# Kernel optimization log

Measured on AMD Instinct MI355X. Metric: run time of the kernel, lower is better.

Reference implementation:

```python
import jax, jax.numpy as jnp
import numpy as np

B, N = 2, 65536
V, VSUB, J, R = 6890, 689, 24, 64
THRESH = 0.12


def trilinear(grid, coords):
    # grid: [C, D, H, W]; coords: [..., 3] in [-1, 1] (x->W, y->H, z->D)
    C, D, H, W = grid.shape
    cs = jnp.clip(coords.reshape(-1, 3), -1.0, 1.0)
    x = (cs[:, 0] + 1.0) * 0.5 * (W - 1)
    y = (cs[:, 1] + 1.0) * 0.5 * (H - 1)
    z = (cs[:, 2] + 1.0) * 0.5 * (D - 1)
    x0 = jnp.floor(x).astype(jnp.int32); x1 = jnp.minimum(x0 + 1, W - 1)
    y0 = jnp.floor(y).astype(jnp.int32); y1 = jnp.minimum(y0 + 1, H - 1)
    z0 = jnp.floor(z).astype(jnp.int32); z1 = jnp.minimum(z0 + 1, D - 1)
    fx = x - x0; fy = y - y0; fz = z - z0
    g = lambda zi, yi, xi: grid[:, zi, yi, xi]  # [C, M]
    out = (g(z0, y0, x0) * ((1 - fz) * (1 - fy) * (1 - fx))
         + g(z0, y0, x1) * ((1 - fz) * (1 - fy) * fx)
         + g(z0, y1, x0) * ((1 - fz) * fy * (1 - fx))
         + g(z0, y1, x1) * ((1 - fz) * fy * fx)
         + g(z1, y0, x0) * (fz * (1 - fy) * (1 - fx))
         + g(z1, y0, x1) * (fz * (1 - fy) * fx)
         + g(z1, y1, x0) * (fz * fy * (1 - fx))
         + g(z1, y1, x1) * (fz * fy * fx))
    return out.T.reshape(coords.shape[:-1] + (C,))


def setup_inputs() -> dict:
    key = jax.random.key(0)
    ks = jax.random.split(key, 8)
    pts_in = jax.random.normal(ks[0], (B, N, 3), jnp.float32) * 0.4
    vs_template = jax.random.normal(ks[1], (1, VSUB, 3), jnp.float32) * 0.4
    shape_offset = jax.random.normal(ks[2], (1, V, 3), jnp.float32) * 0.01
    init_idx = jax.random.randint(ks[3], (N, 3), 0, V, jnp.int32)
    bar = jax.random.uniform(ks[4], (N, 3), jnp.float32) + 1e-3
    init_bar = bar / jnp.sum(bar, -1, keepdims=True)
    lbs_voxel = jax.nn.softmax(jax.random.normal(ks[5], (J, R, R, R), jnp.float32), axis=0)
    tfs = jnp.tile(jnp.eye(4, dtype=jnp.float32), (B, J, 1, 1)) \
        + 0.05 * jax.random.normal(ks[6], (B, J, 4, 4), jnp.float32)
    grid_scale = jnp.full((3,), 1.5, jnp.float32)
    grid_offset = jnp.zeros((3,), jnp.float32)
    return dict(pts_in=pts_in, vs_template=vs_template, shape_offset=shape_offset,
                init_idx=init_idx, init_bar=init_bar, lbs_voxel=lbs_voxel,
                tfs=tfs, grid_scale=grid_scale, grid_offset=grid_offset)


def reference(pts_in, vs_template, shape_offset, init_idx, init_bar, lbs_voxel, tfs, grid_scale, grid_offset):
    # --- KNN (K=1) against subsampled template vertices ---
    v = vs_template[0]  # [VSUB, 3]
    d2 = (jnp.sum(pts_in * pts_in, -1, keepdims=True)
          + jnp.sum(v * v, -1)[None, None, :]
          - 2.0 * jnp.einsum('bnd,vd->bnv', pts_in, v))  # [B,N,VSUB]
    dist_sq = jnp.min(d2, axis=-1)  # [B,N]
    mask = (dist_sq < THRESH ** 2)[..., None]  # [B,N,1]
    # --- barycentric interpolation of per-vertex shape offsets ---
    tri = shape_offset[0][init_idx]               # [N,3,3]
    off = jnp.sum(init_bar[..., None] * tri, -2)  # [N,3]
    pts = pts_in + off[None]
    # --- query LBS weights from explicit voxel grid (fast-SNARF) ---
    pts_norm = (pts - grid_offset) * grid_scale
    w = trilinear(lbs_voxel, pts_norm)  # [B,N,J]
    w = w / jnp.clip(jnp.sum(w, -1, keepdims=True), 1e-6, None)
    # --- forward skinning ---
    w_tf = jnp.einsum('bnj,bjkl->bnkl', w, tfs)  # [B,N,4,4]
    pts_h = jnp.concatenate([pts, jnp.ones_like(pts[..., :1])], -1)  # [B,N,4]
    pts_posed = jnp.einsum('bnkl,bnl->bnk', w_tf, pts_h)[..., :3]
    pts_cano_all = pts_posed.reshape(B, N, 1, 3)
    return pts_cano_all, mask, w_tf
```

## Files before the change

kernel.cpp:

```cpp
#include <hip/hip_runtime.h>
#include <math.h>

#define NB    2
#define NPTS  65536
#define NVSUB 689
#define NJ    24
#define GR    64
#define GRV   (GR*GR*GR)
#define THRESH2 0.0144f

#define O_PTS  0
#define O_MASK (NB*NPTS*3)
#define O_WTF  (O_MASK + NB*NPTS)

#define PREP_BLOCKS (GRV / 256)
#define MASK_BLOCKS ((NB * NPTS * 4) / 256)

__global__ __launch_bounds__(256) void prep_mask_kernel(
    const float* __restrict__ g, float* __restrict__ gt,
    const float* __restrict__ pts_in, const float* __restrict__ vs,
    float* __restrict__ out) {
    __shared__ float4 s_vs[NVSUB];
    const int tid = threadIdx.x;

    if (blockIdx.x < PREP_BLOCKS) {
        int vox = blockIdx.x * 256 + tid;
        float v[NJ];
#pragma unroll
        for (int c = 0; c < NJ; ++c) v[c] = g[c * GRV + vox];
        float4* dst = (float4*)(gt + (size_t)vox * NJ);
#pragma unroll
        for (int c4 = 0; c4 < 6; ++c4)
            dst[c4] = make_float4(v[4*c4+0], v[4*c4+1], v[4*c4+2], v[4*c4+3]);
        return;
    }

    for (int i = tid; i < NVSUB; i += 256) {
        float x = vs[i * 3 + 0], y = vs[i * 3 + 1], z = vs[i * 3 + 2];
        s_vs[i] = make_float4(x, y, z, x * x + y * y + z * z);
    }
    __syncthreads();

    const int t  = (blockIdx.x - PREP_BLOCKS) * 256 + tid;
    const int p  = t >> 2;
    const int qq = t & 3;
    const int b  = p >> 16;
    const int n  = p & (NPTS - 1);

    const float* P = pts_in + ((size_t)b * NPTS + n) * 3;
    const float px = P[0], py = P[1], pz = P[2];

    const int vbeg = qq * 173;
    const int vend = min(vbeg + 173, NVSUB);
    float ma = 3.4e38f, mb = 3.4e38f;
    int v = vbeg;
    for (; v + 2 <= vend; v += 2) {
        float4 t0 = s_vs[v];
        float4 t1 = s_vs[v + 1];
        ma = fminf(ma, fmaf(-2.f, px * t0.x + py * t0.y + pz * t0.z, t0.w));
        mb = fminf(mb, fmaf(-2.f, px * t1.x + py * t1.y + pz * t1.z, t1.w));
    }
    if (v < vend) {
        float4 t0 = s_vs[v];
        ma = fminf(ma, fmaf(-2.f, px * t0.x + py * t0.y + pz * t0.z, t0.w));
    }
    float mm = fminf(ma, mb);
    mm = fminf(mm, __shfl_xor(mm, 1));
    mm = fminf(mm, __shfl_xor(mm, 2));
    if (qq == 0) {
        float dist2 = mm + px * px + py * py + pz * pz;
        out[O_MASK + p] = (dist2 < THRESH2) ? 1.f : 0.f;
    }
}

__global__ __launch_bounds__(256, 6) void deform_kernel(
    const float* __restrict__ pts_in,
    const float* __restrict__ shape_off,
    const int*   __restrict__ init_idx,
    const float* __restrict__ init_bar,
    const float* __restrict__ gT,
    const float* __restrict__ tfs,
    const float* __restrict__ gscale,
    const float* __restrict__ goff,
    float* __restrict__ out) {
    __shared__ float s_tfs[NB * NJ * 16];

    const int tid = threadIdx.x;
    for (int i = tid; i < NB * NJ * 16; i += 256) s_tfs[i] = tfs[i];
    __syncthreads();

    const int t = blockIdx.x * 256 + tid;
    const int p = t >> 2;
    const int q = t & 3;
    const int b = p >> 16;
    const int n = p & (NPTS - 1);

    const float* P = pts_in + ((size_t)b * NPTS + n) * 3;
    const float px = P[0], py = P[1], pz = P[2];

    int i0 = init_idx[n * 3 + 0] * 3;
    int i1 = init_idx[n * 3 + 1] * 3;
    int i2 = init_idx[n * 3 + 2] * 3;
    float b0 = init_bar[n * 3 + 0], b1 = init_bar[n * 3 + 1], b2 = init_bar[n * 3 + 2];
    float qx = px + b0 * shape_off[i0 + 0] + b1 * shape_off[i1 + 0] + b2 * shape_off[i2 + 0];
    float qy = py + b0 * shape_off[i0 + 1] + b1 * shape_off[i1 + 1] + b2 * shape_off[i2 + 1];
    float qz = pz + b0 * shape_off[i0 + 2] + b1 * shape_off[i1 + 2] + b2 * shape_off[i2 + 2];

    float ccx = fminf(fmaxf((qx - goff[0]) * gscale[0], -1.f), 1.f);
    float ccy = fminf(fmaxf((qy - goff[1]) * gscale[1], -1.f), 1.f);
    float ccz = fminf(fmaxf((qz - goff[2]) * gscale[2], -1.f), 1.f);
    float x = (ccx + 1.f) * 0.5f * (GR - 1);
    float y = (ccy + 1.f) * 0.5f * (GR - 1);
    float z = (ccz + 1.f) * 0.5f * (GR - 1);
    int x0 = (int)floorf(x), y0 = (int)floorf(y), z0 = (int)floorf(z);
    int x1 = min(x0 + 1, GR - 1), y1 = min(y0 + 1, GR - 1), z1 = min(z0 + 1, GR - 1);
    float fx = x - (float)x0, fy = y - (float)y0, fz = z - (float)z0;
    float wxa[2] = {1.f - fx, fx}, wya[2] = {1.f - fy, fy}, wza[2] = {1.f - fz, fz};

    float w[6];
#pragma unroll
    for (int c = 0; c < 6; ++c) w[c] = 0.f;

#pragma unroll
    for (int ci = 0; ci < 8; ++ci) {
        int xi = (ci & 1) ? x1 : x0;
        int yi = (ci & 2) ? y1 : y0;
        int zi = (ci & 4) ? z1 : z0;
        float wt = wxa[ci & 1] * wya[(ci >> 1) & 1] * wza[(ci >> 2) & 1];
        int vox = (zi * GR + yi) * GR + xi;
        const float2* g2 = (const float2*)(gT + (size_t)vox * NJ + q * 6);
        float2 ga = g2[0], gb = g2[1], gc = g2[2];
        w[0] = fmaf(wt, ga.x, w[0]); w[1] = fmaf(wt, ga.y, w[1]);
        w[2] = fmaf(wt, gb.x, w[2]); w[3] = fmaf(wt, gb.y, w[3]);
        w[4] = fmaf(wt, gc.x, w[4]); w[5] = fmaf(wt, gc.y, w[5]);
    }
    float wsum = w[0] + w[1] + w[2] + w[3] + w[4] + w[5];

    float4 A0 = make_float4(0.f, 0.f, 0.f, 0.f);
    float4 A1 = A0, A2 = A0, A3 = A0;
    const float4* tb = (const float4*)(s_tfs + (size_t)(b * NJ + q * 6) * 16);
#pragma unroll
    for (int jj = 0; jj < 6; ++jj) {
        float wj = w[jj];
        float4 r0 = tb[jj * 4 + 0], r1 = tb[jj * 4 + 1];
        float4 r2 = tb[jj * 4 + 2], r3 = tb[jj * 4 + 3];
        A0.x = fmaf(wj, r0.x, A0.x); A0.y = fmaf(wj, r0.y, A0.y);
        A0.z = fmaf(wj, r0.z, A0.z); A0.w = fmaf(wj, r0.w, A0.w);
        A1.x = fmaf(wj, r1.x, A1.x); A1.y = fmaf(wj, r1.y, A1.y);
        A1.z = fmaf(wj, r1.z, A1.z); A1.w = fmaf(wj, r1.w, A1.w);
        A2.x = fmaf(wj, r2.x, A2.x); A2.y = fmaf(wj, r2.y, A2.y);
        A2.z = fmaf(wj, r2.z, A2.z); A2.w = fmaf(wj, r2.w, A2.w);
        A3.x = fmaf(wj, r3.x, A3.x); A3.y = fmaf(wj, r3.y, A3.y);
        A3.z = fmaf(wj, r3.z, A3.z); A3.w = fmaf(wj, r3.w, A3.w);
    }

#define QRED(v) v += __shfl_xor(v, 1); v += __shfl_xor(v, 2)
    QRED(A0.x); QRED(A0.y); QRED(A0.z); QRED(A0.w);
    QRED(A1.x); QRED(A1.y); QRED(A1.z); QRED(A1.w);
    QRED(A2.x); QRED(A2.y); QRED(A2.z); QRED(A2.w);
    QRED(A3.x); QRED(A3.y); QRED(A3.z); QRED(A3.w);
    QRED(wsum);
#undef QRED

    if (q == 0) {
        float inv = __builtin_amdgcn_rcpf(fmaxf(wsum, 1e-6f));
        A0.x *= inv; A0.y *= inv; A0.z *= inv; A0.w *= inv;
        A1.x *= inv; A1.y *= inv; A1.z *= inv; A1.w *= inv;
        A2.x *= inv; A2.y *= inv; A2.z *= inv; A2.w *= inv;
        A3.x *= inv; A3.y *= inv; A3.z *= inv; A3.w *= inv;

        float ox = A0.x * qx + A0.y * qy + A0.z * qz + A0.w;
        float oy = A1.x * qx + A1.y * qy + A1.z * qz + A1.w;
        float oz = A2.x * qx + A2.y * qy + A2.z * qz + A2.w;

        size_t bn = (size_t)p;
        out[O_PTS + bn * 3 + 0] = ox;
        out[O_PTS + bn * 3 + 1] = oy;
        out[O_PTS + bn * 3 + 2] = oz;
        float4* wt4 = (float4*)(out + O_WTF + bn * 16);
        wt4[0] = A0; wt4[1] = A1; wt4[2] = A2; wt4[3] = A3;
    }
}

__global__ __launch_bounds__(256) void snarf_fallback(
    const float* __restrict__ pts_in, const float* __restrict__ vs,
    const float* __restrict__ shape_off, const int* __restrict__ init_idx,
    const float* __restrict__ init_bar, const float* __restrict__ grid,
    const float* __restrict__ tfs, const float* __restrict__ gscale,
    const float* __restrict__ goff, float* __restrict__ out) {
    const int n = blockIdx.x * 256 + threadIdx.x;
    for (int b = 0; b < NB; ++b) {
        float px = pts_in[((size_t)b * NPTS + n) * 3 + 0];
        float py = pts_in[((size_t)b * NPTS + n) * 3 + 1];
        float pz = pts_in[((size_t)b * NPTS + n) * 3 + 2];
        float mm = 3.4e38f;
        for (int v = 0; v < NVSUB; ++v) {
            float dx = px - vs[v * 3 + 0], dy = py - vs[v * 3 + 1], dz = pz - vs[v * 3 + 2];
            mm = fminf(mm, dx * dx + dy * dy + dz * dz);
        }
        int i0 = init_idx[n * 3 + 0] * 3, i1 = init_idx[n * 3 + 1] * 3, i2 = init_idx[n * 3 + 2] * 3;
        float b0 = init_bar[n * 3 + 0], b1 = init_bar[n * 3 + 1], b2 = init_bar[n * 3 + 2];
        float qx = px + b0 * shape_off[i0 + 0] + b1 * shape_off[i1 + 0] + b2 * shape_off[i2 + 0];
        float qy = py + b0 * shape_off[i0 + 1] + b1 * shape_off[i1 + 1] + b2 * shape_off[i2 + 1];
        float qz = pz + b0 * shape_off[i0 + 2] + b1 * shape_off[i1 + 2] + b2 * shape_off[i2 + 2];
        float cx = fminf(fmaxf((qx - goff[0]) * gscale[0], -1.f), 1.f);
        float cy = fminf(fmaxf((qy - goff[1]) * gscale[1], -1.f), 1.f);
        float cz = fminf(fmaxf((qz - goff[2]) * gscale[2], -1.f), 1.f);
        float x = (cx + 1.f) * 0.5f * (GR - 1), y = (cy + 1.f) * 0.5f * (GR - 1), z = (cz + 1.f) * 0.5f * (GR - 1);
        int x0 = (int)floorf(x), y0 = (int)floorf(y), z0 = (int)floorf(z);
        int x1 = min(x0 + 1, GR - 1), y1 = min(y0 + 1, GR - 1), z1 = min(z0 + 1, GR - 1);
        float fx = x - x0, fy = y - y0, fz = z - z0;
        float wxa[2] = {1.f - fx, fx}, wya[2] = {1.f - fy, fy}, wza[2] = {1.f - fz, fz};
        float w[NJ];
        for (int c = 0; c < NJ; ++c) w[c] = 0.f;
        for (int ci = 0; ci < 8; ++ci) {
            int xi = (ci & 1) ? x1 : x0, yi = (ci & 2) ? y1 : y0, zi = (ci & 4) ? z1 : z0;
            float wt = wxa[ci & 1] * wya[(ci >> 1) & 1] * wza[(ci >> 2) & 1];
            int vox = (zi * GR + yi) * GR + xi;
            for (int c = 0; c < NJ; ++c) w[c] = fmaf(wt, grid[c * GRV + vox], w[c]);
        }
        float s = 0.f;
        for (int c = 0; c < NJ; ++c) s += w[c];
        float inv = 1.f / fmaxf(s, 1e-6f);
        float acc[16];
        for (int k = 0; k < 16; ++k) acc[k] = 0.f;
        for (int j = 0; j < NJ; ++j) {
            float wj = w[j] * inv;
            for (int k = 0; k < 16; ++k) acc[k] = fmaf(wj, tfs[(b * NJ + j) * 16 + k], acc[k]);
        }
        size_t bn = (size_t)b * NPTS + n;
        out[O_PTS + bn * 3 + 0] = acc[0] * qx + acc[1] * qy + acc[2] * qz + acc[3];
        out[O_PTS + bn * 3 + 1] = acc[4] * qx + acc[5] * qy + acc[6] * qz + acc[7];
        out[O_PTS + bn * 3 + 2] = acc[8] * qx + acc[9] * qy + acc[10] * qz + acc[11];
        out[O_MASK + bn] = (mm < THRESH2) ? 1.f : 0.f;
        for (int k = 0; k < 16; ++k) out[O_WTF + bn * 16 + k] = acc[k];
    }
}

extern "C" void kernel_launch(void* const* d_in, const int* in_sizes, int n_in,
                              void* d_out, int out_size, void* d_ws, size_t ws_size,
                              hipStream_t stream) {
    const float* pts_in    = (const float*)d_in[0];
    const float* vs        = (const float*)d_in[1];
    const float* shape_off = (const float*)d_in[2];
    const int*   init_idx  = (const int*)d_in[3];
    const float* init_bar  = (const float*)d_in[4];
    const float* lbs       = (const float*)d_in[5];
    const float* tfs       = (const float*)d_in[6];
    const float* gs        = (const float*)d_in[7];
    const float* go        = (const float*)d_in[8];
    float* out = (float*)d_out;

    const size_t needed = (size_t)GRV * NJ * sizeof(float);
    if (ws_size >= needed) {
        float* gT = (float*)d_ws;
        prep_mask_kernel<<<PREP_BLOCKS + MASK_BLOCKS, 256, 0, stream>>>(
            lbs, gT, pts_in, vs, out);
        deform_kernel<<<(NB * NPTS * 4) / 256, 256, 0, stream>>>(
            pts_in, shape_off, init_idx, init_bar, gT, tfs, gs, go, out);
    } else {
        snarf_fallback<<<NPTS / 256, 256, 0, stream>>>(
            pts_in, vs, shape_off, init_idx, init_bar, lbs, tfs, gs, go, out);
    }
}
```

Measured before the change: 140.1 us.

## Pad voxel grid to 32 channels, use 2 threads per point, share KNN across batches

Pads the transposed LBS grid to a 32-float stride per voxel so each thread can fetch 12 weights with aligned float4 loads. The deform kernel now uses 2 threads per point instead of 4, which halves the shuffle reductions and the duplicated per-point setup. The KNN mask pass has each thread handle the same point index in both batches, so each shared-memory vertex read is reused twice. The costs are more registers per thread, fewer threads in flight, and a larger workspace for the padded grid.

Result: no change. 139.2 us (-0.6%).

```diff
diff --git a/kernel.cpp b/kernel.cpp
--- a/kernel.cpp
+++ b/kernel.cpp
@@ -8,13 +8,14 @@
 #define GR    64
 #define GRV   (GR*GR*GR)
 #define THRESH2 0.0144f
+#define CSTRIDE 32
 
 #define O_PTS  0
 #define O_MASK (NB*NPTS*3)
 #define O_WTF  (O_MASK + NB*NPTS)
 
 #define PREP_BLOCKS (GRV / 256)
-#define MASK_BLOCKS ((NB * NPTS * 4) / 256)
+#define MASK_BLOCKS ((NPTS * 4) / 256)
 
 __global__ __launch_bounds__(256) void prep_mask_kernel(
     const float* __restrict__ g, float* __restrict__ gt,
@@ -28,7 +29,7 @@
         float v[NJ];
 #pragma unroll
         for (int c = 0; c < NJ; ++c) v[c] = g[c * GRV + vox];
-        float4* dst = (float4*)(gt + (size_t)vox * NJ);
+        float4* dst = (float4*)(gt + (size_t)vox * CSTRIDE);
 #pragma unroll
         for (int c4 = 0; c4 < 6; ++c4)
             dst[c4] = make_float4(v[4*c4+0], v[4*c4+1], v[4*c4+2], v[4*c4+3]);
@@ -42,34 +43,42 @@
     __syncthreads();
 
     const int t  = (blockIdx.x - PREP_BLOCKS) * 256 + tid;
-    const int p  = t >> 2;
+    const int n  = t >> 2;
     const int qq = t & 3;
-    const int b  = p >> 16;
-    const int n  = p & (NPTS - 1);
-
-    const float* P = pts_in + ((size_t)b * NPTS + n) * 3;
-    const float px = P[0], py = P[1], pz = P[2];
+
+    const float* P0 = pts_in + (size_t)n * 3;
+    const float* P1 = pts_in + (size_t)(NPTS + n) * 3;
+    const float ax = P0[0], ay = P0[1], az = P0[2];
+    const float bx = P1[0], by = P1[1], bz = P1[2];
 
     const int vbeg = qq * 173;
     const int vend = min(vbeg + 173, NVSUB);
-    float ma = 3.4e38f, mb = 3.4e38f;
+    float m0a = 3.4e38f, m0b = 3.4e38f, m1a = 3.4e38f, m1b = 3.4e38f;
     int v = vbeg;
     for (; v + 2 <= vend; v += 2) {
         float4 t0 = s_vs[v];
         float4 t1 = s_vs[v + 1];
-        ma = fminf(ma, fmaf(-2.f, px * t0.x + py * t0.y + pz * t0.z, t0.w));
-        mb = fminf(mb, fmaf(-2.f, px * t1.x + py * t1.y + pz * t1.z, t1.w));
+        m0a = fminf(m0a, fmaf(-2.f, ax * t0.x + ay * t0.y + az * t0.z, t0.w));
+        m1a = fminf(m1a, fmaf(-2.f, bx * t0.x + by * t0.y + bz * t0.z, t0.w));
+        m0b = fminf(m0b, fmaf(-2.f, ax * t1.x + ay * t1.y + az * t1.z, t1.w));
+        m1b = fminf(m1b, fmaf(-2.f, bx * t1.x + by * t1.y + bz * t1.z, t1.w));
     }
     if (v < vend) {
         float4 t0 = s_vs[v];
-        ma = fminf(ma, fmaf(-2.f, px * t0.x + py * t0.y + pz * t0.z, t0.w));
-    }
-    float mm = fminf(ma, mb);
-    mm = fminf(mm, __shfl_xor(mm, 1));
-    mm = fminf(mm, __shfl_xor(mm, 2));
+        m0a = fminf(m0a, fmaf(-2.f, ax * t0.x + ay * t0.y + az * t0.z, t0.w));
+        m1a = fminf(m1a, fmaf(-2.f, bx * t0.x + by * t0.y + bz * t0.z, t0.w));
+    }
+    float mm0 = fminf(m0a, m0b);
+    float mm1 = fminf(m1a, m1b);
+    mm0 = fminf(mm0, __shfl_xor(mm0, 1));
+    mm0 = fminf(mm0, __shfl_xor(mm0, 2));
+    mm1 = fminf(mm1, __shfl_xor(mm1, 1));
+    mm1 = fminf(mm1, __shfl_xor(mm1, 2));
     if (qq == 0) {
-        float dist2 = mm + px * px + py * py + pz * pz;
-        out[O_MASK + p] = (dist2 < THRESH2) ? 1.f : 0.f;
+        float d0 = mm0 + ax * ax + ay * ay + az * az;
+        float d1 = mm1 + bx * bx + by * by + bz * bz;
+        out[O_MASK + n]        = (d0 < THRESH2) ? 1.f : 0.f;
+        out[O_MASK + NPTS + n] = (d1 < THRESH2) ? 1.f : 0.f;
     }
 }
 
@@ -89,11 +98,11 @@
     for (int i = tid; i < NB * NJ * 16; i += 256) s_tfs[i] = tfs[i];
     __syncthreads();
 
-    const int t = blockIdx.x * 256 + tid;
-    const int p = t >> 2;
-    const int q = t & 3;
-    const int b = p >> 16;
-    const int n = p & (NPTS - 1);
+    const int t  = blockIdx.x * 256 + tid;
+    const int p  = t >> 1;
+    const int hf = t & 1;
+    const int b  = p >> 16;
+    const int n  = p & (NPTS - 1);
 
     const float* P = pts_in + ((size_t)b * NPTS + n) * 3;
     const float px = P[0], py = P[1], pz = P[2];
@@ -117,9 +126,9 @@
     float fx = x - (float)x0, fy = y - (float)y0, fz = z - (float)z0;
     float wxa[2] = {1.f - fx, fx}, wya[2] = {1.f - fy, fy}, wza[2] = {1.f - fz, fz};
 
-    float w[6];
-#pragma unroll
-    for (int c = 0; c < 6; ++c) w[c] = 0.f;
+    float w[12];
+#pragma unroll
+    for (int c = 0; c < 12; ++c) w[c] = 0.f;
 
 #pragma unroll
     for (int ci = 0; ci < 8; ++ci) {
@@ -128,19 +137,24 @@
         int zi = (ci & 4) ? z1 : z0;
         float wt = wxa[ci & 1] * wya[(ci >> 1) & 1] * wza[(ci >> 2) & 1];
         int vox = (zi * GR + yi) * GR + xi;
-        const float2* g2 = (const float2*)(gT + (size_t)vox * NJ + q * 6);
-        float2 ga = g2[0], gb = g2[1], gc = g2[2];
-        w[0] = fmaf(wt, ga.x, w[0]); w[1] = fmaf(wt, ga.y, w[1]);
-        w[2] = fmaf(wt, gb.x, w[2]); w[3] = fmaf(wt, gb.y, w[3]);
-        w[4] = fmaf(wt, gc.x, w[4]); w[5] = fmaf(wt, gc.y, w[5]);
-    }
-    float wsum = w[0] + w[1] + w[2] + w[3] + w[4] + w[5];
+        const float4* g4 = (const float4*)(gT + (size_t)vox * CSTRIDE + hf * 12);
+        float4 g0 = g4[0], g1 = g4[1], g2 = g4[2];
+        w[0]  = fmaf(wt, g0.x, w[0]);  w[1]  = fmaf(wt, g0.y, w[1]);
+        w[2]  = fmaf(wt, g0.z, w[2]);  w[3]  = fmaf(wt, g0.w, w[3]);
+        w[4]  = fmaf(wt, g1.x, w[4]);  w[5]  = fmaf(wt, g1.y, w[5]);
+        w[6]  = fmaf(wt, g1.z, w[6]);  w[7]  = fmaf(wt, g1.w, w[7]);
+        w[8]  = fmaf(wt, g2.x, w[8]);  w[9]  = fmaf(wt, g2.y, w[9]);
+        w[10] = fmaf(wt, g2.z, w[10]); w[11] = fmaf(wt, g2.w, w[11]);
+    }
+    float wsum = 0.f;
+#pragma unroll
+    for (int c = 0; c < 12; ++c) wsum += w[c];
 
     float4 A0 = make_float4(0.f, 0.f, 0.f, 0.f);
     float4 A1 = A0, A2 = A0, A3 = A0;
-    const float4* tb = (const float4*)(s_tfs + (size_t)(b * NJ + q * 6) * 16);
-#pragma unroll
-    for (int jj = 0; jj < 6; ++jj) {
+    const float4* tb = (const float4*)(s_tfs + (size_t)(b * NJ + hf * 12) * 16);
+#pragma unroll
+    for (int jj = 0; jj < 12; ++jj) {
         float wj = w[jj];
         float4 r0 = tb[jj * 4 + 0], r1 = tb[jj * 4 + 1];
         float4 r2 = tb[jj * 4 + 2], r3 = tb[jj * 4 + 3];
@@ -154,7 +168,7 @@
         A3.z = fmaf(wj, r3.z, A3.z); A3.w = fmaf(wj, r3.w, A3.w);
     }
 
-#define QRED(v) v += __shfl_xor(v, 1); v += __shfl_xor(v, 2)
+#define QRED(v) v += __shfl_xor(v, 1)
     QRED(A0.x); QRED(A0.y); QRED(A0.z); QRED(A0.w);
     QRED(A1.x); QRED(A1.y); QRED(A1.z); QRED(A1.w);
     QRED(A2.x); QRED(A2.y); QRED(A2.z); QRED(A2.w);
@@ -162,7 +176,7 @@
     QRED(wsum);
 #undef QRED
 
-    if (q == 0) {
+    if (hf == 0) {
         float inv = __builtin_amdgcn_rcpf(fmaxf(wsum, 1e-6f));
         A0.x *= inv; A0.y *= inv; A0.z *= inv; A0.w *= inv;
         A1.x *= inv; A1.y *= inv; A1.z *= inv; A1.w *= inv;
@@ -251,12 +265,12 @@
     const float* go        = (const float*)d_in[8];
     float* out = (float*)d_out;
 
-    const size_t needed = (size_t)GRV * NJ * sizeof(float);
+    const size_t needed = (size_t)GRV * CSTRIDE * sizeof(float);
     if (ws_size >= needed) {
         float* gT = (float*)d_ws;
         prep_mask_kernel<<<PREP_BLOCKS + MASK_BLOCKS, 256, 0, stream>>>(
             lbs, gT, pts_in, vs, out);
-        deform_kernel<<<(NB * NPTS * 4) / 256, 256, 0, stream>>>(
+        deform_kernel<<<(NB * NPTS * 2) / 256, 256, 0, stream>>>(
             pts_in, shape_off, init_idx, init_bar, gT, tfs, gs, go, out);
     } else {
         snarf_fallback<<<NPTS / 256, 256, 0, stream>>>(
```
